# Kernel optimization log

Measured on AMD Instinct MI355X. Metric: run time of the kernel, lower is better.

The kernel has to match this reference:

```python
import jax, jax.numpy as jnp
import numpy as np


def setup_inputs() -> dict:
    key = jax.random.key(0)
    k = jax.random.split(key, 5)
    bs, n_heads, ch, n_obj, emb = 4, 8, 64, 8, 64
    ih = iw = 32
    T = ih * iw
    return {
        "qkv": jax.random.normal(k[0], (bs, 3 * n_heads * ch, T), dtype=jnp.float32),
        "bboxes": jax.random.uniform(k[1], (bs, n_obj, 5), dtype=jnp.float32),
        "null_prompt_emb": jax.random.normal(k[2], (bs, emb, T), dtype=jnp.float32),
        "prompt_emb": jax.random.normal(k[3], (bs, emb, T), dtype=jnp.float32),
        "W_prompt": jax.random.normal(k[4], (3 * n_heads * ch, emb), dtype=jnp.float32) * 0.02,
        "n_heads": n_heads,
        "image_h": ih,
        "image_w": iw,
    }


def _region_masks(bboxes, h, w):
    # Faithful translation of get_region: bbox unpacked as (x, y, width, height, obj_idx).
    # Returns float masks [b, n_obj, h*w].
    x, y, bw, bh = bboxes[..., 0], bboxes[..., 1], bboxes[..., 2], bboxes[..., 3]
    i0 = jnp.minimum(float(h) - 1.0, jnp.floor(y * h))
    j0 = jnp.minimum(float(w) - 1.0, jnp.floor(x * w))
    i1 = i0 + jnp.maximum(1.0, jnp.ceil(bh * h))
    j1 = j0 + jnp.maximum(1.0, jnp.ceil(bw * w))
    ii = jnp.arange(h, dtype=jnp.float32)
    jj = jnp.arange(w, dtype=jnp.float32)
    mi = (ii >= i0[..., None]) & (ii < i1[..., None])          # [b, n, h]
    mj = (jj >= j0[..., None]) & (jj < j1[..., None])          # [b, n, w]
    m = (mi[..., :, None] & mj[..., None, :]).astype(jnp.float32)  # [b, n, h, w]
    return m.reshape(m.shape[0], m.shape[1], h * w)


def reference(qkv, bboxes, null_prompt_emb, prompt_emb, W_prompt, n_heads, image_h, image_w):
    bs, width, T = qkv.shape
    ch = width // (3 * n_heads)
    scale = float(ch) ** -0.25  # 1/sqrt(sqrt(ch))

    def split3(x):
        x = x.reshape(bs * n_heads, 3 * ch, T)
        return x[:, :ch], x[:, ch:2 * ch], x[:, 2 * ch:]

    q, k, v = split3(qkv)
    # to_prompt_token is a 1x1 Conv1d (no bias) == matmul over the channel dim
    nq, nk, nv = split3(jnp.einsum('oc,bct->bot', W_prompt, null_prompt_emb))
    pq, pk, pv = split3(jnp.einsum('oc,bct->bot', W_prompt, prompt_emb))

    def attn(qh, kh, vh, col_mask=None):
        w = jnp.einsum('bct,bcs->bts', qh * scale, kh * scale)
        if col_mask is not None:
            w = jnp.where(col_mask[:, None, :] > 0.5, w, -1e9)
        w = jax.nn.softmax(w.astype(jnp.float32), axis=-1).astype(qh.dtype)
        return jnp.einsum('bts,bcs->btc', w, vh)  # [bs*heads, T, ch]

    # global (null-prompt) attention
    a_null = attn(q + nq, k + nk, v + nv)

    # per-object masked attention, blended by region masks
    masks = _region_masks(bboxes, image_h, image_w)       # [bs, n_obj, T]
    masks = jnp.repeat(masks, n_heads, axis=0)            # [(bs*heads), n_obj, T]
    qf, kf, vf = q + pq, k + pk, v + pv
    a_fg = jnp.zeros_like(a_null)
    counter = jnp.zeros((bs * n_heads, T, 1), dtype=jnp.float32)
    for o in range(masks.shape[1]):  # small fixed loop over objects
        m = masks[:, o]                                   # [bs*heads, T]
        a_fg = a_fg + m[:, :, None] * attn(qf, kf, vf, col_mask=m)
        counter = counter + m[:, :, None]
    fg = counter > 0.5
    a_final = jnp.where(fg, a_fg, a_null) / jnp.where(fg, counter, 1.0)
    return jnp.transpose(a_final, (0, 2, 1)).reshape(bs, n_heads * ch, T)
```

## Files before the change

kernel.cpp:

```cpp
#include <hip/hip_runtime.h>
#include <math.h>

#define BS 4
#define NH 8
#define TT 1024
#define WROWS 1536
#define NOBJ 8
#define NT 65536

#define QNT_OFF  0
#define KNT_OFF  2097152
#define VNCS_OFF 4194304
#define QFT_OFF  6291456
#define KFT_OFF  8388608
#define VFT_OFF  10485760

typedef __attribute__((ext_vector_type(8))) short short8;
typedef __attribute__((ext_vector_type(4))) float v4f;

#if __has_builtin(__builtin_amdgcn_exp2f)
#define EXP2(x) __builtin_amdgcn_exp2f(x)
#else
#define EXP2(x) exp2f(x)
#endif

__device__ __forceinline__ short f2bf(float f) {
    unsigned u = __float_as_uint(f);
    u = (u + 0x7FFF + ((u >> 16) & 1)) >> 16;
    return (short)u;
}
__device__ __forceinline__ unsigned p2(float a, float b) {
    return (unsigned)(unsigned short)f2bf(a) | ((unsigned)(unsigned short)f2bf(b) << 16);
}
__device__ __forceinline__ unsigned p2t(float a, float b) {
    return (__float_as_uint(a) >> 16) | (__float_as_uint(b) & 0xFFFF0000u);
}

__device__ __forceinline__ void get_region(const float* __restrict__ bb,
                                           int& i0, int& j0, int& hh, int& ww) {
    float x = bb[0], y = bb[1], bw = bb[2], bh = bb[3];
    float i0f = fminf(31.0f, floorf(y * 32.0f));
    float j0f = fminf(31.0f, floorf(x * 32.0f));
    float i1f = i0f + fmaxf(1.0f, ceilf(bh * 32.0f));
    float j1f = j0f + fmaxf(1.0f, ceilf(bw * 32.0f));
    i0 = (int)i0f; j0 = (int)j0f;
    int i1 = min(32, (int)i1f);
    int j1 = min(32, (int)j1f);
    hh = i1 - i0; ww = j1 - j0;
}

__global__ __launch_bounds__(256)
void fuse_kernel(const float* __restrict__ qkv, const float* __restrict__ nEmb,
                 const float* __restrict__ pEmb, const float* __restrict__ W,
                 short* __restrict__ wsS) {
    __shared__ float WtT[64][68];
    __shared__ float En[64][64];
    __shared__ float Ep[64][64];
    short* sbufA = (short*)&WtT[0][0];
    short* sbufB = (short*)&En[0][0];
    int t0 = blockIdx.x * 64;
    int r0 = blockIdx.y * 64;
    int b  = blockIdx.z;
    int tid = threadIdx.x;
    int half = tid >> 4;
    int q4 = (tid & 15) * 4;
    int tr = tid >> 4, tc = tid & 15;
    float4 xq[4];
#pragma unroll
    for (int i = 0; i < 4; ++i)
        xq[i] = *(const float4*)&qkv[(b * WROWS + r0 + tr * 4 + i) * TT + t0 + tc * 4];
#pragma unroll
    for (int p = 0; p < 4; ++p) {
        int rr = p * 16 + half;
        float4 w4 = *(const float4*)&W[(r0 + rr) * 64 + q4];
        WtT[q4 + 0][rr] = w4.x; WtT[q4 + 1][rr] = w4.y;
        WtT[q4 + 2][rr] = w4.z; WtT[q4 + 3][rr] = w4.w;
        int e = p * 16 + half;
        *(float4*)&En[e][q4] = *(const float4*)&nEmb[(b * 64 + e) * TT + t0 + q4];
        *(float4*)&Ep[e][q4] = *(const float4*)&pEmb[(b * 64 + e) * TT + t0 + q4];
    }
    __syncthreads();
    float an[4][4] = {{0.f}}, ap[4][4] = {{0.f}};
#pragma unroll 8
    for (int e = 0; e < 64; ++e) {
        float4 w4 = *(const float4*)&WtT[e][tr * 4];
        float4 n4 = *(const float4*)&En[e][tc * 4];
        float4 p4 = *(const float4*)&Ep[e][tc * 4];
        float w[4]  = {w4.x, w4.y, w4.z, w4.w};
        float nn[4] = {n4.x, n4.y, n4.z, n4.w};
        float pp[4] = {p4.x, p4.y, p4.z, p4.w};
#pragma unroll
        for (int i = 0; i < 4; ++i)
#pragma unroll
            for (int j = 0; j < 4; ++j) {
                an[i][j] += w[i] * nn[j];
                ap[i][j] += w[i] * pp[j];
            }
    }
    int sec = (r0 % 192) / 64;
    int h = r0 / 192, bh = b * 8 + h;
    float sc = (sec == 0) ? 0.18033688f : 1.0f;
#pragma unroll
    for (int i = 0; i < 4; ++i) {
        float4 x4 = xq[i];
        an[i][0] = (an[i][0] + x4.x) * sc; an[i][1] = (an[i][1] + x4.y) * sc;
        an[i][2] = (an[i][2] + x4.z) * sc; an[i][3] = (an[i][3] + x4.w) * sc;
        ap[i][0] = (ap[i][0] + x4.x) * sc; ap[i][1] = (ap[i][1] + x4.y) * sc;
        ap[i][2] = (ap[i][2] + x4.z) * sc; ap[i][3] = (ap[i][3] + x4.w) * sc;
    }
    if (sec == 2) {
        short* Vn = wsS + VNCS_OFF + bh * NT;
#pragma unroll
        for (int i = 0; i < 4; ++i) {
            int c = tr * 4 + i;
            uint2 pk; pk.x = p2(an[i][0], an[i][1]); pk.y = p2(an[i][2], an[i][3]);
            *(uint2*)&Vn[c * TT + t0 + tc * 4] = pk;
        }
        short* dst = wsS + VFT_OFF + bh * NT + t0 * 64;
        __syncthreads();
#pragma unroll
        for (int i = 0; i < 4; ++i)
#pragma unroll
            for (int j = 0; j < 4; ++j)
                sbufB[(tc * 4 + j) * 72 + tr * 4 + i] = f2bf(ap[i][j]);
        __syncthreads();
#pragma unroll
        for (int rep = 0; rep < 2; ++rep) {
            int idx = rep * 256 + tid; int tl = idx >> 3, c8 = idx & 7;
            *(short8*)&dst[tl * 64 + c8 * 8] = *(const short8*)&sbufB[tl * 72 + c8 * 8];
        }
    } else {
        short* dn = wsS + (sec == 0 ? QNT_OFF : KNT_OFF) + bh * NT + t0 * 64;
        short* df = wsS + (sec == 0 ? QFT_OFF : KFT_OFF) + bh * NT + t0 * 64;
        __syncthreads();
#pragma unroll
        for (int i = 0; i < 4; ++i)
#pragma unroll
            for (int j = 0; j < 4; ++j) {
                sbufA[(tc * 4 + j) * 72 + tr * 4 + i] = f2bf(an[i][j]);
                sbufB[(tc * 4 + j) * 72 + tr * 4 + i] = f2bf(ap[i][j]);
            }
        __syncthreads();
#pragma unroll
        for (int rep = 0; rep < 2; ++rep) {
            int idx = rep * 256 + tid; int tl = idx >> 3, c8 = idx & 7;
            *(short8*)&dn[tl * 64 + c8 * 8] = *(const short8*)&sbufA[tl * 72 + c8 * 8];
            *(short8*)&df[tl * 64 + c8 * 8] = *(const short8*)&sbufB[tl * 72 + c8 * 8];
        }
    }
}

__global__ __launch_bounds__(256)
void attn_fused(const short* __restrict__ wsS, const float* __restrict__ bboxes,
                float* __restrict__ out) {
    __shared__ __align__(16) short lds[13824];
    __shared__ unsigned short tmap[1024];
    short* Qs = lds;
    short* Ks = lds + 4608;
    short* Vs = lds + 9216;
    int bh = blockIdx.x, rt = blockIdx.y;
    int b = bh >> 3, h = bh & 7;
    int t0 = rt * 64;
    int tid = threadIdx.x;
    int w = tid >> 6, lane = tid & 63, ln = lane & 15, qd = lane >> 4;
    const short* QnT = wsS + QNT_OFF + bh * NT;
    const short* KnT = wsS + KNT_OFF + bh * NT;
    const short* Vn  = wsS + VNCS_OFF + bh * NT;
    const short* QfT = wsS + QFT_OFF + bh * NT;
    const short* KfT = wsS + KFT_OFF + bh * NT;
    const short* VfT = wsS + VFT_OFF + bh * NT;

    int r0i = 2 * rt, r1i = 2 * rt + 1;
    unsigned inter = 0u, cov0 = 0u, cov1 = 0u;
    for (int o = 0; o < NOBJ; ++o) {
        int i0, j0, hh, ww;
        get_region(&bboxes[(b * NOBJ + o) * 5], i0, j0, hh, ww);
        int i1 = i0 + hh;
        if (i0 <= r1i && i1 > r0i) {
            inter |= (1u << o);
            unsigned wm = (ww >= 32) ? 0xFFFFFFFFu : (((1u << ww) - 1u) << j0);
            if (i0 <= r0i && r0i < i1) cov0 |= wm;
            if (i0 <= r1i && r1i < i1) cov1 |= wm;
        }
    }

    v4f Onull[4];
#pragma unroll
    for (int cc = 0; cc < 4; ++cc) Onull[cc] = (v4f){0.f, 0.f, 0.f, 0.f};

    if ((cov0 & cov1) != 0xFFFFFFFFu) {
#pragma unroll
        for (int rep = 0; rep < 2; ++rep) {
            int idx = rep * 256 + tid; int cell = idx >> 3, o8 = idx & 7;
            *(short8*)&Qs[cell * 72 + o8 * 8] =
                *(const short8*)&QnT[(t0 + cell) * 64 + o8 * 8];
        }
        __syncthreads();
        short8 aq0 = *(const short8*)&Qs[(16 * w + ln) * 72 + qd * 8];
        short8 aq1 = *(const short8*)&Qs[(16 * w + ln) * 72 + 32 + qd * 8];
        v4f O[4]; float l[4];
#pragma unroll
        for (int r = 0; r < 4; ++r) l[r] = 0.f;
#pragma unroll
        for (int cc = 0; cc < 4; ++cc) O[cc] = (v4f){0.f, 0.f, 0.f, 0.f};
        short8 kreg[2], vreg[2];
#pragma unroll
        for (int rep = 0; rep < 2; ++rep) {
            int idx = rep * 256 + tid; int cell = idx >> 3, o8 = idx & 7;
            int pc = 4 * (cell & 15) + (cell >> 4);
            kreg[rep] = *(const short8*)&KnT[pc * 64 + o8 * 8];
            vreg[rep] = *(const short8*)&Vn[cell * TT + o8 * 8];
        }
        for (int ct = 0; ct < 16; ++ct) {
            __syncthreads();
#pragma unroll
            for (int rep = 0; rep < 2; ++rep) {
                int idx = rep * 256 + tid; int cell = idx >> 3, o8 = idx & 7;
                *(short8*)&Ks[cell * 72 + o8 * 8] = kreg[rep];
                *(short8*)&Vs[cell * 72 + o8 * 8] = vreg[rep];
            }
            __syncthreads();
            if (ct < 15) {
                int s0 = (ct + 1) * 64;
#pragma unroll
                for (int rep = 0; rep < 2; ++rep) {
                    int idx = rep * 256 + tid; int cell = idx >> 3, o8 = idx & 7;
                    int pc = 4 * (cell & 15) + (cell >> 4);
                    kreg[rep] = *(const short8*)&KnT[(s0 + pc) * 64 + o8 * 8];
                    vreg[rep] = *(const short8*)&Vn[cell * TT + s0 + o8 * 8];
                }
            }
            v4f S[4];
#pragma unroll
            for (int nn = 0; nn < 4; ++nn) {
                short8 b0 = *(const short8*)&Ks[(nn * 16 + ln) * 72 + qd * 8];
                short8 b1 = *(const short8*)&Ks[(nn * 16 + ln) * 72 + 32 + qd * 8];
                v4f z = (v4f){0.f, 0.f, 0.f, 0.f};
                z = __builtin_amdgcn_mfma_f32_16x16x32_bf16(aq0, b0, z, 0, 0, 0);
                z = __builtin_amdgcn_mfma_f32_16x16x32_bf16(aq1, b1, z, 0, 0, 0);
                S[nn] = z;
            }
#pragma unroll
            for (int r = 0; r < 4; ++r) {
                float e0 = EXP2(S[0][r]);
                float e1 = EXP2(S[1][r]);
                float e2 = EXP2(S[2][r]);
                float e3 = EXP2(S[3][r]);
                l[r] += e0 + e1 + e2 + e3;
                uint2 pk; pk.x = p2t(e0, e1); pk.y = p2t(e2, e3);
                *(uint2*)&Qs[(w * 16 + 4 * qd + r) * 72 + 4 * ln] = pk;
            }
            short8 ap0 = *(const short8*)&Qs[(w * 16 + ln) * 72 + qd * 8];
            short8 ap1 = *(const short8*)&Qs[(w * 16 + ln) * 72 + 32 + qd * 8];
#pragma unroll
            for (int cc = 0; cc < 4; ++cc) {
                short8 bv0 = *(const short8*)&Vs[(cc * 16 + ln) * 72 + qd * 8];
                short8 bv1 = *(const short8*)&Vs[(cc * 16 + ln) * 72 + 32 + qd * 8];
                O[cc] = __builtin_amdgcn_mfma_f32_16x16x32_bf16(ap0, bv0, O[cc], 0, 0, 0);
                O[cc] = __builtin_amdgcn_mfma_f32_16x16x32_bf16(ap1, bv1, O[cc], 0, 0, 0);
            }
        }
#pragma unroll
        for (int r = 0; r < 4; ++r) {
            float rs = l[r];
            rs += __shfl_xor(rs, 1, 64);
            rs += __shfl_xor(rs, 2, 64);
            rs += __shfl_xor(rs, 4, 64);
            rs += __shfl_xor(rs, 8, 64);
            float inv = 1.0f / rs;
#pragma unroll
            for (int cc = 0; cc < 4; ++cc) Onull[cc][r] = O[cc][r] * inv;
        }
    }

    v4f Oacc[4]; float cnt[4];
#pragma unroll
    for (int r = 0; r < 4; ++r) cnt[r] = 0.f;
#pragma unroll
    for (int cc = 0; cc < 4; ++cc) Oacc[cc] = (v4f){0.f, 0.f, 0.f, 0.f};

    if (inter != 0u) {
        __syncthreads();
#pragma unroll
        for (int rep = 0; rep < 2; ++rep) {
            int idx = rep * 256 + tid; int cell = idx >> 3, o8 = idx & 7;
            *(short8*)&Qs[cell * 72 + o8 * 8] =
                *(const short8*)&QfT[(t0 + cell) * 64 + o8 * 8];
        }
        __syncthreads();
        short8 aq0 = *(const short8*)&Qs[(16 * w + ln) * 72 + qd * 8];
        short8 aq1 = *(const short8*)&Qs[(16 * w + ln) * 72 + 32 + qd * 8];
        for (int o = 0; o < NOBJ; ++o) {
            if (!((inter >> o) & 1u)) continue;
            int i0, j0, hh, ww;
            get_region(&bboxes[(b * NOBJ + o) * 5], i0, j0, hh, ww);
            int i1 = i0 + hh;
            int R = hh * ww;
            for (int idx = tid; idx < R; idx += 256) {
                int ri = idx / ww; int rj = idx - ri * ww;
                tmap[idx] = (unsigned short)((i0 + ri) * 32 + j0 + rj);
            }
            __syncthreads();
            v4f O[4]; float l[4];
#pragma unroll
            for (int r = 0; r < 4; ++r) l[r] = 0.f;
#pragma unroll
            for (int cc = 0; cc < 4; ++cc) O[cc] = (v4f){0.f, 0.f, 0.f, 0.f};
            int nct = (R + 63) >> 6;
            short8 kreg[2], vreg[2];
#pragma unroll
            for (int rep = 0; rep < 2; ++rep) {
                int idx = rep * 256 + tid; int cell = idx >> 3, o8 = idx & 7;
                int pc = 4 * (cell & 15) + (cell >> 4);
                int tk = tmap[min(pc, R - 1)];
                int tv = tmap[min(cell, R - 1)];
                kreg[rep] = *(const short8*)&KfT[tk * 64 + o8 * 8];
                vreg[rep] = *(const short8*)&VfT[tv * 64 + o8 * 8];
            }
            for (int ct = 0; ct < nct; ++ct) {
                int sb = ct * 64;
                __syncthreads();
#pragma unroll
                for (int rep = 0; rep < 2; ++rep) {
                    int idx = rep * 256 + tid; int cell = idx >> 3, o8 = idx & 7;
                    *(short8*)&Ks[cell * 72 + o8 * 8] = kreg[rep];
#pragma unroll
                    for (int jj = 0; jj < 8; ++jj) {
                        int j = (jj + o8) & 7;
                        Vs[(o8 * 8 + j) * 72 + cell] = vreg[rep][j];
                    }
                }
                __syncthreads();
                if (ct + 1 < nct) {
                    int s0 = sb + 64;
#pragma unroll
                    for (int rep = 0; rep < 2; ++rep) {
                        int idx = rep * 256 + tid; int cell = idx >> 3, o8 = idx & 7;
                        int pc = 4 * (cell & 15) + (cell >> 4);
                        int tk = tmap[min(s0 + pc, R - 1)];
                        int tv = tmap[min(s0 + cell, R - 1)];
                        kreg[rep] = *(const short8*)&KfT[tk * 64 + o8 * 8];
                        vreg[rep] = *(const short8*)&VfT[tv * 64 + o8 * 8];
                    }
                }
                v4f S[4];
#pragma unroll
                for (int nn = 0; nn < 4; ++nn) {
                    short8 b0 = *(const short8*)&Ks[(nn * 16 + ln) * 72 + qd * 8];
                    short8 b1 = *(const short8*)&Ks[(nn * 16 + ln) * 72 + 32 + qd * 8];
                    v4f z = (v4f){0.f, 0.f, 0.f, 0.f};
                    z = __builtin_amdgcn_mfma_f32_16x16x32_bf16(aq0, b0, z, 0, 0, 0);
                    z = __builtin_amdgcn_mfma_f32_16x16x32_bf16(aq1, b1, z, 0, 0, 0);
                    S[nn] = z;
                }
                float v0 = (sb + 4 * ln + 0) < R ? 1.f : 0.f;
                float v1 = (sb + 4 * ln + 1) < R ? 1.f : 0.f;
                float v2 = (sb + 4 * ln + 2) < R ? 1.f : 0.f;
                float v3 = (sb + 4 * ln + 3) < R ? 1.f : 0.f;
#pragma unroll
                for (int r = 0; r < 4; ++r) {
                    float e0 = EXP2(S[0][r]) * v0;
                    float e1 = EXP2(S[1][r]) * v1;
                    float e2 = EXP2(S[2][r]) * v2;
                    float e3 = EXP2(S[3][r]) * v3;
                    l[r] += e0 + e1 + e2 + e3;
                    uint2 pk; pk.x = p2t(e0, e1); pk.y = p2t(e2, e3);
                    *(uint2*)&Qs[(w * 16 + 4 * qd + r) * 72 + 4 * ln] = pk;
                }
                short8 ap0 = *(const short8*)&Qs[(w * 16 + ln) * 72 + qd * 8];
                short8 ap1 = *(const short8*)&Qs[(w * 16 + ln) * 72 + 32 + qd * 8];
#pragma unroll
                for (int cc = 0; cc < 4; ++cc) {
                    short8 bv0 = *(const short8*)&Vs[(cc * 16 + ln) * 72 + qd * 8];
                    short8 bv1 = *(const short8*)&Vs[(cc * 16 + ln) * 72 + 32 + qd * 8];
                    O[cc] = __builtin_amdgcn_mfma_f32_16x16x32_bf16(ap0, bv0, O[cc], 0, 0, 0);
                    O[cc] = __builtin_amdgcn_mfma_f32_16x16x32_bf16(ap1, bv1, O[cc], 0, 0, 0);
                }
            }
#pragma unroll
            for (int r = 0; r < 4; ++r) {
                float rs = l[r];
                rs += __shfl_xor(rs, 1, 64);
                rs += __shfl_xor(rs, 2, 64);
                rs += __shfl_xor(rs, 4, 64);
                rs += __shfl_xor(rs, 8, 64);
                float inv = 1.0f / rs;
                int t = t0 + 16 * w + 4 * qd + r;
                int ti = t >> 5, tj = t & 31;
                bool in = (ti >= i0) && (ti < i1) && (tj >= j0) && (tj < j0 + ww);
                if (in) {
                    cnt[r] += 1.f;
#pragma unroll
                    for (int cc = 0; cc < 4; ++cc) Oacc[cc][r] += O[cc][r] * inv;
                }
            }
        }
    }

    __syncthreads();
    float* Ot = (float*)lds;
#pragma unroll
    for (int r = 0; r < 4; ++r) {
        int tl = 16 * w + 4 * qd + r;
        float icnt = cnt[r] > 0.f ? 1.0f / cnt[r] : 0.f;
#pragma unroll
        for (int cc = 0; cc < 4; ++cc) {
            float val = cnt[r] > 0.f ? Oacc[cc][r] * icnt : Onull[cc][r];
            Ot[(cc * 16 + ln) * 68 + tl] = val;
        }
    }
    __syncthreads();
    int obase = (b * 512 + h * 64) * TT + t0;
#pragma unroll
    for (int rep = 0; rep < 4; ++rep) {
        int idx = rep * 256 + tid; int c = idx >> 4, t4 = (idx & 15) * 4;
        *(float4*)&out[obase + c * TT + t4] = *(float4*)&Ot[c * 68 + t4];
    }
}

extern "C" void kernel_launch(void* const* d_in, const int* in_sizes, int n_in,
                              void* d_out, int out_size, void* d_ws, size_t ws_size,
                              hipStream_t stream) {
    const float* qkv    = (const float*)d_in[0];
    const float* bboxes = (const float*)d_in[1];
    const float* nEmb   = (const float*)d_in[2];
    const float* pEmb   = (const float*)d_in[3];
    const float* W      = (const float*)d_in[4];
    short* wsS = (short*)d_ws;
    float* out = (float*)d_out;

    fuse_kernel<<<dim3(16, 24, 4), 256, 0, stream>>>(qkv, nEmb, pEmb, W, wsS);
    attn_fused<<<dim3(32, 16), 256, 0, stream>>>(wsS, bboxes, out);
}
```

Before: 162.1 us.

## Split object-masked attention into per-object query-compact blocks with atomic accumulation

Restructures the attention kernel so each object gets its own grid slice (z dimension). Each block processes a 64-row tile of that object's compacted region queries, not scanning every object for every 64-query image tile. Per-object results are scaled by 1/count and atomically added into a zero-initialised output. The null-attention slice writes only uncovered positions. This removes the serial per-object loop in each block and the wasted work on query rows outside the object region. In exchange it adds a memset, float atomics with order-dependent rounding, and recomputation of the coverage count per row.

```diff
diff --git a/kernel.cpp b/kernel.cpp
--- a/kernel.cpp
+++ b/kernel.cpp
@@ -151,44 +151,158 @@
 }
 
 __global__ __launch_bounds__(256)
-void attn_fused(const short* __restrict__ wsS, const float* __restrict__ bboxes,
-                float* __restrict__ out) {
+void attn_pc(const short* __restrict__ wsS, const float* __restrict__ bboxes,
+             float* __restrict__ out) {
     __shared__ __align__(16) short lds[13824];
     __shared__ unsigned short tmap[1024];
     short* Qs = lds;
     short* Ks = lds + 4608;
     short* Vs = lds + 9216;
-    int bh = blockIdx.x, rt = blockIdx.y;
+    int bh = blockIdx.x, rt = blockIdx.y, z = blockIdx.z;
     int b = bh >> 3, h = bh & 7;
-    int t0 = rt * 64;
     int tid = threadIdx.x;
     int w = tid >> 6, lane = tid & 63, ln = lane & 15, qd = lane >> 4;
-    const short* QnT = wsS + QNT_OFF + bh * NT;
-    const short* KnT = wsS + KNT_OFF + bh * NT;
-    const short* Vn  = wsS + VNCS_OFF + bh * NT;
-    const short* QfT = wsS + QFT_OFF + bh * NT;
-    const short* KfT = wsS + KFT_OFF + bh * NT;
-    const short* VfT = wsS + VFT_OFF + bh * NT;
-
-    int r0i = 2 * rt, r1i = 2 * rt + 1;
-    unsigned inter = 0u, cov0 = 0u, cov1 = 0u;
-    for (int o = 0; o < NOBJ; ++o) {
+    int obase = (b * 512 + h * 64) * TT;
+
+    if (z < 8) {
+        int o = z;
         int i0, j0, hh, ww;
         get_region(&bboxes[(b * NOBJ + o) * 5], i0, j0, hh, ww);
-        int i1 = i0 + hh;
-        if (i0 <= r1i && i1 > r0i) {
-            inter |= (1u << o);
+        int R = hh * ww;
+        if (rt * 64 >= R) return;
+        const short* QfT = wsS + QFT_OFF + bh * NT;
+        const short* KfT = wsS + KFT_OFF + bh * NT;
+        const short* VfT = wsS + VFT_OFF + bh * NT;
+        for (int idx = tid; idx < R; idx += 256) {
+            int ri = idx / ww; int rj = idx - ri * ww;
+            tmap[idx] = (unsigned short)((i0 + ri) * 32 + j0 + rj);
+        }
+        __syncthreads();
+#pragma unroll
+        for (int rep = 0; rep < 2; ++rep) {
+            int idx = rep * 256 + tid; int cell = idx >> 3, o8 = idx & 7;
+            int rq = min(rt * 64 + cell, R - 1);
+            *(short8*)&Qs[cell * 72 + o8 * 8] =
+                *(const short8*)&QfT[tmap[rq] * 64 + o8 * 8];
+        }
+        __syncthreads();
+        short8 aq0 = *(const short8*)&Qs[(16 * w + ln) * 72 + qd * 8];
+        short8 aq1 = *(const short8*)&Qs[(16 * w + ln) * 72 + 32 + qd * 8];
+        v4f O[4]; float l[4];
+#pragma unroll
+        for (int r = 0; r < 4; ++r) l[r] = 0.f;
+#pragma unroll
+        for (int cc = 0; cc < 4; ++cc) O[cc] = (v4f){0.f, 0.f, 0.f, 0.f};
+        int nct = (R + 63) >> 6;
+        short8 kreg[2], vreg[2];
+#pragma unroll
+        for (int rep = 0; rep < 2; ++rep) {
+            int idx = rep * 256 + tid; int cell = idx >> 3, o8 = idx & 7;
+            int pc = 4 * (cell & 15) + (cell >> 4);
+            int tk = tmap[min(pc, R - 1)];
+            int tv = tmap[min(cell, R - 1)];
+            kreg[rep] = *(const short8*)&KfT[tk * 64 + o8 * 8];
+            vreg[rep] = *(const short8*)&VfT[tv * 64 + o8 * 8];
+        }
+        for (int ct = 0; ct < nct; ++ct) {
+            int sb = ct * 64;
+            __syncthreads();
+#pragma unroll
+            for (int rep = 0; rep < 2; ++rep) {
+                int idx = rep * 256 + tid; int cell = idx >> 3, o8 = idx & 7;
+                *(short8*)&Ks[cell * 72 + o8 * 8] = kreg[rep];
+#pragma unroll
+                for (int jj = 0; jj < 8; ++jj) {
+                    int j = (jj + o8) & 7;
+                    Vs[(o8 * 8 + j) * 72 + cell] = vreg[rep][j];
+                }
+            }
+            __syncthreads();
+            if (ct + 1 < nct) {
+                int s0 = sb + 64;
+#pragma unroll
+                for (int rep = 0; rep < 2; ++rep) {
+                    int idx = rep * 256 + tid; int cell = idx >> 3, o8 = idx & 7;
+                    int pc = 4 * (cell & 15) + (cell >> 4);
+                    int tk = tmap[min(s0 + pc, R - 1)];
+                    int tv = tmap[min(s0 + cell, R - 1)];
+                    kreg[rep] = *(const short8*)&KfT[tk * 64 + o8 * 8];
+                    vreg[rep] = *(const short8*)&VfT[tv * 64 + o8 * 8];
+                }
+            }
+            v4f S[4];
+#pragma unroll
+            for (int nn = 0; nn < 4; ++nn) {
+                short8 b0 = *(const short8*)&Ks[(nn * 16 + ln) * 72 + qd * 8];
+                short8 b1 = *(const short8*)&Ks[(nn * 16 + ln) * 72 + 32 + qd * 8];
+                v4f zz = (v4f){0.f, 0.f, 0.f, 0.f};
+                zz = __builtin_amdgcn_mfma_f32_16x16x32_bf16(aq0, b0, zz, 0, 0, 0);
+                zz = __builtin_amdgcn_mfma_f32_16x16x32_bf16(aq1, b1, zz, 0, 0, 0);
+                S[nn] = zz;
+            }
+            float v0 = (sb + 4 * ln + 0) < R ? 1.f : 0.f;
+            float v1 = (sb + 4 * ln + 1) < R ? 1.f : 0.f;
+            float v2 = (sb + 4 * ln + 2) < R ? 1.f : 0.f;
+            float v3 = (sb + 4 * ln + 3) < R ? 1.f : 0.f;
+#pragma unroll
+            for (int r = 0; r < 4; ++r) {
+                float e0 = EXP2(S[0][r]) * v0;
+                float e1 = EXP2(S[1][r]) * v1;
+                float e2 = EXP2(S[2][r]) * v2;
+                float e3 = EXP2(S[3][r]) * v3;
+                l[r] += e0 + e1 + e2 + e3;
+                uint2 pk; pk.x = p2t(e0, e1); pk.y = p2t(e2, e3);
+                *(uint2*)&Qs[(w * 16 + 4 * qd + r) * 72 + 4 * ln] = pk;
+            }
+            short8 ap0 = *(const short8*)&Qs[(w * 16 + ln) * 72 + qd * 8];
+            short8 ap1 = *(const short8*)&Qs[(w * 16 + ln) * 72 + 32 + qd * 8];
+#pragma unroll
+            for (int cc = 0; cc < 4; ++cc) {
+                short8 bv0 = *(const short8*)&Vs[(cc * 16 + ln) * 72 + qd * 8];
+                short8 bv1 = *(const short8*)&Vs[(cc * 16 + ln) * 72 + 32 + qd * 8];
+                O[cc] = __builtin_amdgcn_mfma_f32_16x16x32_bf16(ap0, bv0, O[cc], 0, 0, 0);
+                O[cc] = __builtin_amdgcn_mfma_f32_16x16x32_bf16(ap1, bv1, O[cc], 0, 0, 0);
+            }
+        }
+#pragma unroll
+        for (int r = 0; r < 4; ++r) {
+            int rg = rt * 64 + 16 * w + 4 * qd + r;
+            if (rg >= R) continue;
+            float rs = l[r];
+            rs += __shfl_xor(rs, 1, 64);
+            rs += __shfl_xor(rs, 2, 64);
+            rs += __shfl_xor(rs, 4, 64);
+            rs += __shfl_xor(rs, 8, 64);
+            int t = tmap[rg];
+            int ti = t >> 5, tj = t & 31;
+            int cnt = 0;
+#pragma unroll
+            for (int oo = 0; oo < NOBJ; ++oo) {
+                int ii0, jj0, hh2, ww2;
+                get_region(&bboxes[(b * NOBJ + oo) * 5], ii0, jj0, hh2, ww2);
+                if (ti >= ii0 && ti < ii0 + hh2 && tj >= jj0 && tj < jj0 + ww2) cnt++;
+            }
+            float coeff = 1.0f / (rs * (float)cnt);
+#pragma unroll
+            for (int cc = 0; cc < 4; ++cc)
+                unsafeAtomicAdd(&out[obase + (cc * 16 + ln) * TT + t], O[cc][r] * coeff);
+        }
+    } else {
+        int r0i = 2 * rt, r1i = 2 * rt + 1;
+        unsigned cov0 = 0u, cov1 = 0u;
+        for (int o = 0; o < NOBJ; ++o) {
+            int i0, j0, hh, ww;
+            get_region(&bboxes[(b * NOBJ + o) * 5], i0, j0, hh, ww);
+            int i1 = i0 + hh;
             unsigned wm = (ww >= 32) ? 0xFFFFFFFFu : (((1u << ww) - 1u) << j0);
             if (i0 <= r0i && r0i < i1) cov0 |= wm;
             if (i0 <= r1i && r1i < i1) cov1 |= wm;
         }
-    }
-
-    v4f Onull[4];
-#pragma unroll
-    for (int cc = 0; cc < 4; ++cc) Onull[cc] = (v4f){0.f, 0.f, 0.f, 0.f};
-
-    if ((cov0 & cov1) != 0xFFFFFFFFu) {
+        if ((cov0 & cov1) == 0xFFFFFFFFu) return;
+        int t0 = rt * 64;
+        const short* QnT = wsS + QNT_OFF + bh * NT;
+        const short* KnT = wsS + KNT_OFF + bh * NT;
+        const short* Vn  = wsS + VNCS_OFF + bh * NT;
 #pragma unroll
         for (int rep = 0; rep < 2; ++rep) {
             int idx = rep * 256 + tid; int cell = idx >> 3, o8 = idx & 7;
@@ -235,10 +349,10 @@
             for (int nn = 0; nn < 4; ++nn) {
                 short8 b0 = *(const short8*)&Ks[(nn * 16 + ln) * 72 + qd * 8];
                 short8 b1 = *(const short8*)&Ks[(nn * 16 + ln) * 72 + 32 + qd * 8];
-                v4f z = (v4f){0.f, 0.f, 0.f, 0.f};
-                z = __builtin_amdgcn_mfma_f32_16x16x32_bf16(aq0, b0, z, 0, 0, 0);
-                z = __builtin_amdgcn_mfma_f32_16x16x32_bf16(aq1, b1, z, 0, 0, 0);
-                S[nn] = z;
+                v4f zz = (v4f){0.f, 0.f, 0.f, 0.f};
+                zz = __builtin_amdgcn_mfma_f32_16x16x32_bf16(aq0, b0, zz, 0, 0, 0);
+                zz = __builtin_amdgcn_mfma_f32_16x16x32_bf16(aq1, b1, zz, 0, 0, 0);
+                S[nn] = zz;
             }
 #pragma unroll
             for (int r = 0; r < 4; ++r) {
@@ -269,152 +383,29 @@
             rs += __shfl_xor(rs, 8, 64);
             float inv = 1.0f / rs;
 #pragma unroll
-            for (int cc = 0; cc < 4; ++cc) Onull[cc][r] = O[cc][r] * inv;
-        }
-    }
-
-    v4f Oacc[4]; float cnt[4];
-#pragma unroll
-    for (int r = 0; r < 4; ++r) cnt[r] = 0.f;
-#pragma unroll
-    for (int cc = 0; cc < 4; ++cc) Oacc[cc] = (v4f){0.f, 0.f, 0.f, 0.f};
-
-    if (inter != 0u) {
-        __syncthreads();
-#pragma unroll
-        for (int rep = 0; rep < 2; ++rep) {
-            int idx = rep * 256 + tid; int cell = idx >> 3, o8 = idx & 7;
-            *(short8*)&Qs[cell * 72 + o8 * 8] =
-                *(const short8*)&QfT[(t0 + cell) * 64 + o8 * 8];
-        }
-        __syncthreads();
-        short8 aq0 = *(const short8*)&Qs[(16 * w + ln) * 72 + qd * 8];
-        short8 aq1 = *(const short8*)&Qs[(16 * w + ln) * 72 + 32 + qd * 8];
-        for (int o = 0; o < NOBJ; ++o) {
-            if (!((inter >> o) & 1u)) continue;
-            int i0, j0, hh, ww;
-            get_region(&bboxes[(b * NOBJ + o) * 5], i0, j0, hh, ww);
-            int i1 = i0 + hh;
-            int R = hh * ww;
-            for (int idx = tid; idx < R; idx += 256) {
-                int ri = idx / ww; int rj = idx - ri * ww;
-                tmap[idx] = (unsigned short)((i0 + ri) * 32 + j0 + rj);
-            }
-            __syncthreads();
-            v4f O[4]; float l[4];
-#pragma unroll
-            for (int r = 0; r < 4; ++r) l[r] = 0.f;
-#pragma unroll
-            for (int cc = 0; cc < 4; ++cc) O[cc] = (v4f){0.f, 0.f, 0.f, 0.f};
-            int nct = (R + 63) >> 6;
-            short8 kreg[2], vreg[2];
-#pragma unroll
-            for (int rep = 0; rep < 2; ++rep) {
-                int idx = rep * 256 + tid; int cell = idx >> 3, o8 = idx & 7;
-                int pc = 4 * (cell & 15) + (cell >> 4);
-                int tk = tmap[min(pc, R - 1)];
-                int tv = tmap[min(cell, R - 1)];
-                kreg[rep] = *(const short8*)&KfT[tk * 64 + o8 * 8];
-                vreg[rep] = *(const short8*)&VfT[tv * 64 + o8 * 8];
-            }
-            for (int ct = 0; ct < nct; ++ct) {
-                int sb = ct * 64;
-                __syncthreads();
-#pragma unroll
-                for (int rep = 0; rep < 2; ++rep) {
-                    int idx = rep * 256 + tid; int cell = idx >> 3, o8 = idx & 7;
-                    *(short8*)&Ks[cell * 72 + o8 * 8] = kreg[rep];
-#pragma unroll
-                    for (int jj = 0; jj < 8; ++jj) {
-                        int j = (jj + o8) & 7;
-                        Vs[(o8 * 8 + j) * 72 + cell] = vreg[rep][j];
-                    }
-                }
-                __syncthreads();
-                if (ct + 1 < nct) {
-                    int s0 = sb + 64;
-#pragma unroll
-                    for (int rep = 0; rep < 2; ++rep) {
-                        int idx = rep * 256 + tid; int cell = idx >> 3, o8 = idx & 7;
-                        int pc = 4 * (cell & 15) + (cell >> 4);
-                        int tk = tmap[min(s0 + pc, R - 1)];
-                        int tv = tmap[min(s0 + cell, R - 1)];
-                        kreg[rep] = *(const short8*)&KfT[tk * 64 + o8 * 8];
-                        vreg[rep] = *(const short8*)&VfT[tv * 64 + o8 * 8];
-                    }
-                }
-                v4f S[4];
-#pragma unroll
-                for (int nn = 0; nn < 4; ++nn) {
-                    short8 b0 = *(const short8*)&Ks[(nn * 16 + ln) * 72 + qd * 8];
-                    short8 b1 = *(const short8*)&Ks[(nn * 16 + ln) * 72 + 32 + qd * 8];
-                    v4f z = (v4f){0.f, 0.f, 0.f, 0.f};
-                    z = __builtin_amdgcn_mfma_f32_16x16x32_bf16(aq0, b0, z, 0, 0, 0);
-                    z = __builtin_amdgcn_mfma_f32_16x16x32_bf16(aq1, b1, z, 0, 0, 0);
-                    S[nn] = z;
-                }
-                float v0 = (sb + 4 * ln + 0) < R ? 1.f : 0.f;
-                float v1 = (sb + 4 * ln + 1) < R ? 1.f : 0.f;
-                float v2 = (sb + 4 * ln + 2) < R ? 1.f : 0.f;
-                float v3 = (sb + 4 * ln + 3) < R ? 1.f : 0.f;
-#pragma unroll
-                for (int r = 0; r < 4; ++r) {
-                    float e0 = EXP2(S[0][r]) * v0;
-                    float e1 = EXP2(S[1][r]) * v1;
-                    float e2 = EXP2(S[2][r]) * v2;
-                    float e3 = EXP2(S[3][r]) * v3;
-                    l[r] += e0 + e1 + e2 + e3;
-                    uint2 pk; pk.x = p2t(e0, e1); pk.y = p2t(e2, e3);
-                    *(uint2*)&Qs[(w * 16 + 4 * qd + r) * 72 + 4 * ln] = pk;
-                }
-                short8 ap0 = *(const short8*)&Qs[(w * 16 + ln) * 72 + qd * 8];
-                short8 ap1 = *(const short8*)&Qs[(w * 16 + ln) * 72 + 32 + qd * 8];
-#pragma unroll
-                for (int cc = 0; cc < 4; ++cc) {
-                    short8 bv0 = *(const short8*)&Vs[(cc * 16 + ln) * 72 + qd * 8];
-                    short8 bv1 = *(const short8*)&Vs[(cc * 16 + ln) * 72 + 32 + qd * 8];
-                    O[cc] = __builtin_amdgcn_mfma_f32_16x16x32_bf16(ap0, bv0, O[cc], 0, 0, 0);
-                    O[cc] = __builtin_amdgcn_mfma_f32_16x16x32_bf16(ap1, bv1, O[cc], 0, 0, 0);
-                }
-            }
-#pragma unroll
-            for (int r = 0; r < 4; ++r) {
-                float rs = l[r];
-                rs += __shfl_xor(rs, 1, 64);
-                rs += __shfl_xor(rs, 2, 64);
-                rs += __shfl_xor(rs, 4, 64);
-                rs += __shfl_xor(rs, 8, 64);
-                float inv = 1.0f / rs;
-                int t = t0 + 16 * w + 4 * qd + r;
-                int ti = t >> 5, tj = t & 31;
-                bool in = (ti >= i0) && (ti < i1) && (tj >= j0) && (tj < j0 + ww);
-                if (in) {
-                    cnt[r] += 1.f;
-#pragma unroll
-                    for (int cc = 0; cc < 4; ++cc) Oacc[cc][r] += O[cc][r] * inv;
-                }
-            }
-        }
-    }
-
-    __syncthreads();
-    float* Ot = (float*)lds;
-#pragma unroll
-    for (int r = 0; r < 4; ++r) {
-        int tl = 16 * w + 4 * qd + r;
-        float icnt = cnt[r] > 0.f ? 1.0f / cnt[r] : 0.f;
-#pragma unroll
-        for (int cc = 0; cc < 4; ++cc) {
-            float val = cnt[r] > 0.f ? Oacc[cc][r] * icnt : Onull[cc][r];
-            Ot[(cc * 16 + ln) * 68 + tl] = val;
-        }
-    }
-    __syncthreads();
-    int obase = (b * 512 + h * 64) * TT + t0;
-#pragma unroll
-    for (int rep = 0; rep < 4; ++rep) {
-        int idx = rep * 256 + tid; int c = idx >> 4, t4 = (idx & 15) * 4;
-        *(float4*)&out[obase + c * TT + t4] = *(float4*)&Ot[c * 68 + t4];
+            for (int cc = 0; cc < 4; ++cc) O[cc][r] *= inv;
+        }
+        __syncthreads();
+        float* Ot = (float*)lds;
+#pragma unroll
+        for (int r = 0; r < 4; ++r) {
+            int tl = 16 * w + 4 * qd + r;
+#pragma unroll
+            for (int cc = 0; cc < 4; ++cc)
+                Ot[(cc * 16 + ln) * 68 + tl] = O[cc][r];
+        }
+        __syncthreads();
+#pragma unroll
+        for (int rep = 0; rep < 4; ++rep) {
+            int idx = rep * 256 + tid; int c = idx >> 4, t4 = (idx & 15) * 4;
+#pragma unroll
+            for (int j = 0; j < 4; ++j) {
+                int tl = t4 + j;
+                unsigned cv = (tl < 32) ? cov0 : cov1;
+                if (!((cv >> (tl & 31)) & 1u))
+                    out[obase + t0 + c * TT + tl] = Ot[c * 68 + tl];
+            }
+        }
     }
 }
 
@@ -429,6 +420,7 @@
     short* wsS = (short*)d_ws;
     float* out = (float*)d_out;
 
+    hipMemsetAsync(out, 0, (size_t)BS * 512 * TT * sizeof(float), stream);
     fuse_kernel<<<dim3(16, 24, 4), 256, 0, stream>>>(qkv, nEmb, pEmb, W, wsS);
-    attn_fused<<<dim3(32, 16), 256, 0, stream>>>(wsS, bboxes, out);
-}
+    attn_pc<<<dim3(32, 16, 9), 256, 0, stream>>>(wsS, bboxes, out);
+}
```

Result: slower. 192.1 us (+18.5%).
